# Performance work log

Measured on AMD Instinct MI355X. Metric: run time of the kernel, lower is better.

Reference implementation:

```python
import jax, jax.numpy as jnp
import numpy as np

B, N, E, Dh, L = 64, 128, 1024, 300, 2  # batch, num_utter, emb_dim, hidden_dim, gnn_layers


def gru_cell(x, h, wih, whh, bih, bhh):
    # torch.nn.GRUCell math; gate order r, z, n
    gi = x @ wih.T + bih
    gh = h @ whh.T + bhh
    ir, iz, inn = jnp.split(gi, 3, axis=-1)
    hr, hz, hn = jnp.split(gh, 3, axis=-1)
    r = jax.nn.sigmoid(ir + hr)
    z = jax.nn.sigmoid(iz + hz)
    n = jnp.tanh(inn + r * hn)
    return (1.0 - z) * n + z * h


def dag_layer(Hl, mask, wg, bg, cwih, cwhh, cbih, cbhh, pwih, pwhh, pbih, pbhh):
    # Hl: (B,N,Dh); mask: (B,N,N) strict-causal DAG adjacency (float 0/1)
    wq, wk = wg[:Dh], wg[Dh:]  # GatLinear: Linear(2*Dh, 1) split over [Q; K]
    x0 = Hl[:, 0]
    z0 = jnp.zeros_like(x0)
    C0 = gru_cell(x0, z0, cwih, cwhh, cbih, cbhh)  # grus_c(H0, hx=None)
    P0 = gru_cell(z0, x0, pwih, pwhh, pbih, pbhh)  # grus_p(M=0, H0)
    buf0 = jnp.zeros_like(Hl).at[:, 0].set(C0 + P0)

    xs = (jnp.swapaxes(Hl[:, 1:], 0, 1),      # (N-1,B,Dh)
          jnp.swapaxes(mask[:, 1:], 0, 1),    # (N-1,B,N)
          jnp.arange(1, Hl.shape[1]))

    def step(buf, inp):
        x, m, i = inp  # x:(B,Dh), m:(B,N) allows only positions j<i with adj==1
        alpha = (x @ wq)[:, None] + buf @ wk + bg        # (B,N) additive score
        alpha = alpha - (1.0 - m) * 1e30                 # mask_logic
        w = jax.nn.softmax(alpha, axis=-1)
        M = jnp.einsum('bn,bnd->bd', w, buf)             # attn_sum over history H1
        C = gru_cell(x, M, cwih, cwhh, cbih, cbhh)       # grus_c(H_i, M)
        P = gru_cell(M, x, pwih, pwhh, pbih, pbhh)       # grus_p(M, H_i)
        return buf.at[:, i].set(C + P), None

    buf, _ = jax.lax.scan(step, buf0, xs)
    return buf


def setup_inputs():
    key = jax.random.key(0)
    ks = jax.random.split(key, 16)
    features = jax.random.normal(ks[0], (B, N, E), jnp.float32)
    adj = jax.random.randint(ks[1], (B, N, N), 0, 2, dtype=jnp.int32)
    idx = jnp.arange(1, N)
    adj = adj.at[:, idx, idx - 1].set(1)  # every utterance links to its predecessor (valid DAG)
    s_mask = jax.random.randint(ks[2], (B, N, N), 0, 2, dtype=jnp.int32)
    s_mask_onehot = jax.nn.one_hot(s_mask, 2, dtype=jnp.int32)
    lengths = jnp.full((B,), N, dtype=jnp.int32)
    s = 0.05
    return {
        'features': features,
        'fc1_w': jax.random.normal(ks[3], (E, Dh), jnp.float32) * s,
        'fc1_b': jnp.zeros((Dh,), jnp.float32),
        'gat_w': jax.random.normal(ks[4], (L, 2 * Dh), jnp.float32) * s,
        'gat_b': jnp.zeros((L,), jnp.float32),
        'gc_wih': jax.random.normal(ks[5], (L, 3 * Dh, Dh), jnp.float32) * s,
        'gc_whh': jax.random.normal(ks[6], (L, 3 * Dh, Dh), jnp.float32) * s,
        'gc_bih': jnp.zeros((L, 3 * Dh), jnp.float32),
        'gc_bhh': jnp.zeros((L, 3 * Dh), jnp.float32),
        'gp_wih': jax.random.normal(ks[7], (L, 3 * Dh, Dh), jnp.float32) * s,
        'gp_whh': jax.random.normal(ks[8], (L, 3 * Dh, Dh), jnp.float32) * s,
        'gp_bih': jnp.zeros((L, 3 * Dh), jnp.float32),
        'gp_bhh': jnp.zeros((L, 3 * Dh), jnp.float32),
        'adj': adj,
        's_mask': s_mask,
        's_mask_onehot': s_mask_onehot,
        'lengths': lengths,
    }


def reference(features, fc1_w, fc1_b, gat_w, gat_b, gc_wih, gc_whh, gc_bih, gc_bhh,
              gp_wih, gp_whh, gp_bih, gp_bhh, adj, s_mask, s_mask_onehot, lengths):
    H0 = jax.nn.relu(features @ fc1_w + fc1_b)                 # (B,N,Dh)
    causal = jnp.tril(jnp.ones((N, N), features.dtype), k=-1)  # strictly past (j<i)
    mask = adj.astype(features.dtype) * causal                 # adj[:, i, :i]
    Hs = [H0]
    Hl = H0
    for l in range(L):
        Hl = dag_layer(Hl, mask, gat_w[l], gat_b[l],
                       gc_wih[l], gc_whh[l], gc_bih[l], gc_bhh[l],
                       gp_wih[l], gp_whh[l], gp_bih[l], gp_bhh[l])
        Hs.append(Hl)
    Hs.append(features)
    # nodal_att_type=None -> attentive_node_features is identity; module returns H
    return jnp.concatenate(Hs, axis=2)  # (B,N,Dh*(L+1)+E)
```

## Files before the change

### kernel.cpp

```cpp
#include <hip/hip_runtime.h>
#include <hip/hip_fp16.h>

#define B_   64
#define NB   128
#define E_   1024
#define DH   300
#define G3   900
#define OUTD 1924
#define SLICES 4
#define PK_STRIDE 1800
#define MROW 160

typedef _Float16 h2raw __attribute__((ext_vector_type(2)));

__device__ __forceinline__ float dot2f(unsigned int m2, unsigned int w, float acc) {
    h2raw a, b;
    __builtin_memcpy(&a, &m2, 4);
    __builtin_memcpy(&b, &w, 4);
    return __builtin_amdgcn_fdot2(a, b, acc, false);
}

__device__ __forceinline__ unsigned int packh2(float x, float y) {
    __half2 h;
    h.x = __float2half_rn(x);
    h.y = __float2half_rn(y);
    unsigned int u;
    __builtin_memcpy(&u, &h, 4);
    return u;
}

__device__ __forceinline__ float sigmoidf_(float x) { return 1.f / (1.f + __expf(-x)); }
__device__ __forceinline__ float tanh_fast(float x) { return 1.f - 2.f / (__expf(2.f * x) + 1.f); }

__global__ __launch_bounds__(256)
void copy_feat(const float* __restrict__ f, float* __restrict__ out) {
    const long id = (long)blockIdx.x * 256 + threadIdx.x;
    const long r = id >> 8;
    const int  c = (int)(id & 255);
    const float4 v = ((const float4*)(f + r * E_))[c];
    ((float4*)(out + r * OUTD + 3 * DH))[c] = v;
}

__global__ __launch_bounds__(256)
void pack2(const float* __restrict__ gc_whh, const float* __restrict__ gp_wih,
           unsigned int* __restrict__ dst) {
    const int id = blockIdx.x * 256 + threadIdx.x;
    if (id >= 2 * 150 * PK_STRIDE) return;
    const int l   = id / (150 * PK_STRIDE);
    const int rem = id % (150 * PK_STRIDE);
    const int kp  = rem / PK_STRIDE;
    const int R   = rem % PK_STRIDE;
    const int mat = R / G3;
    const int o   = R % G3;
    const float* W = (mat ? gp_wih : gc_whh) + (long)l * G3 * DH;
    const float2 v = *(const float2*)(W + (long)o * DH + 2 * kp);
    dst[id] = packh2(v.x, v.y);
}

__global__ __launch_bounds__(256)
void pack_af(const float* __restrict__ src, unsigned int* __restrict__ dst) {
    const long id = (long)blockIdx.x * 256 + threadIdx.x;
    const long r = id >> 9;
    const int kp = (int)(id & 511);
    const float2 v = *(const float2*)(src + r * E_ + 2 * kp);
    dst[id] = packh2(v.x, v.y);
}

__global__ __launch_bounds__(256)
void pack_ah(const float* __restrict__ src, unsigned int* __restrict__ dst) {
    const long id = (long)blockIdx.x * 256 + threadIdx.x;
    const long r = id / 160;
    const int kp = (int)(id % 160);
    unsigned int u = 0u;
    if (kp < 150) {
        const float2 v = *(const float2*)(src + r * OUTD + 2 * kp);
        u = packh2(v.x, v.y);
    }
    dst[id] = u;
}

__global__ __launch_bounds__(256)
void pack_bf(const float* __restrict__ W, unsigned int* __restrict__ dst) {
    const int id = blockIdx.x * 256 + threadIdx.x;
    const int n = id >> 9;
    const int kp = id & 511;
    unsigned int u = 0u;
    if (n < DH) u = packh2(W[(2 * kp) * DH + n], W[(2 * kp + 1) * DH + n]);
    dst[id] = u;
}

__global__ __launch_bounds__(256)
void pack_bw(const float* __restrict__ W, unsigned int* __restrict__ dst) {
    const int id = blockIdx.x * 256 + threadIdx.x;
    const int n = id / 160;
    const int kp = id % 160;
    unsigned int u = 0u;
    if (n < G3 && kp < 150) {
        const float2 v = *(const float2*)(W + (long)n * DH + 2 * kp);
        u = packh2(v.x, v.y);
    }
    dst[id] = u;
}

template<int RELU>
__global__ __launch_bounds__(256)
void gemm_h16(const unsigned int* __restrict__ APK, int ldap,
              const unsigned int* __restrict__ BPK, int ldbp,
              const float* __restrict__ bias,
              float* __restrict__ C, int ldc,
              int N, int KP)
{
    __shared__ __align__(16) unsigned int As[16][132];
    __shared__ __align__(16) unsigned int Bs[16][68];
    const int tid = threadIdx.x;
    const int m0 = blockIdx.y * 128;
    const int n0 = blockIdx.x * 64;
    const int tx = tid & 15, ty = tid >> 4;
    const int am = tid >> 1, ak8 = (tid & 1) * 8;
    const int bn = tid >> 2, bk4 = (tid & 3) * 4;

    float acc[8][4] = {{0.f}};
    const unsigned int* ap = APK + (long)(m0 + am) * ldap + ak8;
    const unsigned int* bp = BPK + (long)(n0 + bn) * ldbp + bk4;

    for (int kp0 = 0; kp0 < KP; kp0 += 16) {
        const uint4 a0 = *(const uint4*)(ap + kp0);
        const uint4 a1 = *(const uint4*)(ap + kp0 + 4);
        const uint4 bq = *(const uint4*)(bp + kp0);
        As[ak8 + 0][am] = a0.x; As[ak8 + 1][am] = a0.y;
        As[ak8 + 2][am] = a0.z; As[ak8 + 3][am] = a0.w;
        As[ak8 + 4][am] = a1.x; As[ak8 + 5][am] = a1.y;
        As[ak8 + 6][am] = a1.z; As[ak8 + 7][am] = a1.w;
        Bs[bk4 + 0][bn] = bq.x; Bs[bk4 + 1][bn] = bq.y;
        Bs[bk4 + 2][bn] = bq.z; Bs[bk4 + 3][bn] = bq.w;
        __syncthreads();
        #pragma unroll
        for (int kp = 0; kp < 16; ++kp) {
            const uint4 aA = *(const uint4*)&As[kp][ty * 8];
            const uint4 aB = *(const uint4*)&As[kp][ty * 8 + 4];
            const uint4 bb = *(const uint4*)&Bs[kp][tx * 4];
            const unsigned int av[8] = {aA.x, aA.y, aA.z, aA.w, aB.x, aB.y, aB.z, aB.w};
            const unsigned int bv[4] = {bb.x, bb.y, bb.z, bb.w};
            #pragma unroll
            for (int ii = 0; ii < 8; ++ii)
                #pragma unroll
                for (int jj = 0; jj < 4; ++jj)
                    acc[ii][jj] = dot2f(av[ii], bv[jj], acc[ii][jj]);
        }
        __syncthreads();
    }

    const int gn0 = n0 + tx * 4;
    #pragma unroll
    for (int ii = 0; ii < 8; ++ii) {
        const int gm = m0 + ty * 8 + ii;
        float* cp = C + (long)gm * ldc + gn0;
        if (gn0 + 3 < N) {
            const float4 bb = *(const float4*)&bias[gn0];
            float4 o;
            o.x = acc[ii][0] + bb.x; o.y = acc[ii][1] + bb.y;
            o.z = acc[ii][2] + bb.z; o.w = acc[ii][3] + bb.w;
            if (RELU) { o.x = fmaxf(o.x, 0.f); o.y = fmaxf(o.y, 0.f); o.z = fmaxf(o.z, 0.f); o.w = fmaxf(o.w, 0.f); }
            *(float4*)cp = o;
        } else if (gn0 < N) {
            for (int jj = 0; jj < 4; ++jj) {
                const int gn = gn0 + jj;
                if (gn < N) {
                    float v = acc[ii][jj] + bias[gn];
                    if (RELU) v = fmaxf(v, 0.f);
                    cp[jj] = v;
                }
            }
        }
    }
}

__global__ __launch_bounds__(512, 2)
void scan9(float* __restrict__ out,
           const float* __restrict__ GIC,
           const float* __restrict__ GHP,
           const unsigned int* __restrict__ PK2L,
           const float* __restrict__ cbhh,
           const float* __restrict__ pbih,
           const int* __restrict__ adj,
           const float* __restrict__ wk,
           unsigned long long* __restrict__ TBL,
           int l)
{
    extern __shared__ unsigned int histp[];
    __shared__ float wsm2[NB];
    __shared__ float betas[NB];
    __shared__ float Mlds[DH];
    __shared__ __align__(16) unsigned int M2[152];
    __shared__ float gmv[456];
    __shared__ float mx2s, S_pres;

    const int tid = threadIdx.x;
    const int lane = tid & 63;
    const int wid = tid >> 6;
    const int b = blockIdx.x & 63;
    const int k = blockIdx.x >> 6;
    const int swk = (k == 3) ? 72 : 76;

    float* outb = out + (long)b * NB * OUTD;
    const float* xcol = outb + l * DH;
    float* ycol = outb + (l + 1) * DH;
    const float* gicb = GIC + (long)b * NB * G3;
    const float* ghpb = GHP + (long)b * NB * G3;
    const int* adjb = adj + b * NB * NB;
    unsigned long long* mb = TBL + (long)b * NB * MROW;
    unsigned int* mb32 = (unsigned int*)mb;

    if (tid < 152) M2[tid] = 0u;

    const int D = 76 * k + ((tid < swk) ? tid : 0);
    const float cb0 = cbhh[D], cb1 = cbhh[DH + D], cb2 = cbhh[2 * DH + D];
    const float pb0 = pbih[D], pb1 = pbih[DH + D], pb2 = pbih[2 * DH + D];
    const float wkD = wk[D];

    const int ROWS = 6 * swk;
    int R;
    {
        const int t = (tid < ROWS) ? tid : 0;
        const int d = t % swk;
        const int r = t / swk;
        R = (r / 3) * G3 + (r % 3) * DH + 76 * k + d;
    }
    unsigned int w[152];
    #pragma unroll
    for (int j = 0; j < 150; ++j) w[j] = PK2L[j * PK_STRIDE + R];
    w[150] = 0u; w[151] = 0u;

    __syncthreads();

    const bool isv = (tid >= 256) && (tid < 406);
    const int vt = tid - 256;

    for (int i = 0; i < NB; ++i) {
        float gi0 = 0, gi1 = 0, gi2 = 0, gp0 = 0, gp1 = 0, gp2 = 0, xi = 0;
        if (tid < swk) {
            const float* gic = gicb + (long)i * G3;
            const float* ghp = ghpb + (long)i * G3;
            gi0 = gic[D]; gi1 = gic[DH + D]; gi2 = gic[2 * DH + D];
            gp0 = ghp[D]; gp1 = ghp[DH + D]; gp2 = ghp[2 * DH + D];
            xi = xcol[(long)i * OUTD + D];
        }
        int a0p = 0, a1p = 0;
        if (wid == 2 && i + 1 < NB) {
            a0p = adjb[(i + 1) * NB + lane];
            a1p = adjb[(i + 1) * NB + 64 + lane];
        }

        if (i > 0) {
            float V0 = 0.f, V1 = 0.f;
            if (wid == 0) {
                const unsigned long long* trow = mb + (long)(i - 1) * MROW;
                const unsigned int tag = (unsigned int)i;
                const bool act = (lane < 8);
                unsigned long long tv = 0;
                while (true) {
                    if (act && (unsigned int)tv != tag)
                        tv = __hip_atomic_load(&trow[152 + lane],
                                               __ATOMIC_RELAXED, __HIP_MEMORY_SCOPE_AGENT);
                    if (__all(!act || (unsigned int)tv == tag)) break;
                }
                float bp = 0.f;
                if (act) {
                    const unsigned int hb = (unsigned int)(tv >> 32);
                    __builtin_memcpy(&bp, &hb, 4);
                }
                bp += __shfl_xor(bp, 1);
                bp += __shfl_xor(bp, 2);
                bp += __shfl_xor(bp, 4);
                if (lane == 0) betas[i - 1] = __shfl(bp, 0);

                unsigned long long d0 = 0, d1 = 0;
                if (lane < 38) {
                    d0 = __hip_atomic_load(&trow[2 * lane],
                                           __ATOMIC_RELAXED, __HIP_MEMORY_SCOPE_AGENT);
                    d1 = __hip_atomic_load(&trow[2 * lane + 1],
                                           __ATOMIC_RELAXED, __HIP_MEMORY_SCOPE_AGENT);
                    uint4 q;
                    q.x = (unsigned int)d0; q.y = (unsigned int)(d0 >> 32);
                    q.z = (unsigned int)d1; q.w = (unsigned int)(d1 >> 32);
                    *(uint4*)&histp[(i - 1) * 152 + 4 * lane] = q;
                }
            } else if (isv) {
                #pragma unroll 4
                for (int j = 0; j + 1 < i; ++j) {
                    const float wj = wsm2[j];
                    const unsigned int u = histp[j * 152 + vt];
                    __half2 h; __builtin_memcpy(&h, &u, 4);
                    V0 = fmaf(wj, __half2float(h.x), V0);
                    V1 = fmaf(wj, __half2float(h.y), V1);
                }
            }
            __syncthreads();

            if (isv) {
                const float beta_new = betas[i - 1];
                const float mxl = mx2s;
                float S = S_pres, e;
                if (beta_new > mxl) {
                    const float sc = __expf(mxl - beta_new);
                    V0 *= sc; V1 *= sc; S *= sc; e = 1.f;
                } else {
                    e = __expf(beta_new - mxl);
                }
                const unsigned int u = histp[(i - 1) * 152 + vt];
                __half2 h; __builtin_memcpy(&h, &u, 4);
                S += e;
                V0 = fmaf(e, __half2float(h.x), V0);
                V1 = fmaf(e, __half2float(h.y), V1);
                const float inv = 1.f / S;
                const float m0 = V0 * inv, m1 = V1 * inv;
                Mlds[2 * vt] = m0;
                Mlds[2 * vt + 1] = m1;
                M2[vt] = packh2(m0, m1);
            }
        } else {
            if (tid < DH) Mlds[tid] = 0.f;
        }
        __syncthreads();

        if (tid < ROWS) {
            float a0 = 0.f, a1 = 0.f;
            #pragma unroll
            for (int j4 = 0; j4 < 152; j4 += 4) {
                const uint4 m4 = *(const uint4*)&M2[j4];
                a0 = dot2f(m4.x, w[j4 + 0], a0);
                a1 = dot2f(m4.y, w[j4 + 1], a1);
                a0 = dot2f(m4.z, w[j4 + 2], a0);
                a1 = dot2f(m4.w, w[j4 + 3], a1);
            }
            gmv[tid] = a0 + a1;
        }
        __syncthreads();

        if (wid < 2) {
            float rowv = 0.f;
            if (tid < swk) {
                const float Mi = Mlds[D];
                const float hc0 = gmv[0 * swk + tid] + cb0;
                const float hc1 = gmv[1 * swk + tid] + cb1;
                const float hc2 = gmv[2 * swk + tid] + cb2;
                const float rc = sigmoidf_(gi0 + hc0);
                const float zc = sigmoidf_(gi1 + hc1);
                const float nc = tanh_fast(gi2 + rc * hc2);
                const float Cc = (1.f - zc) * nc + zc * Mi;
                const float ip0 = gmv[3 * swk + tid] + pb0;
                const float ip1 = gmv[4 * swk + tid] + pb1;
                const float ip2 = gmv[5 * swk + tid] + pb2;
                const float rp = sigmoidf_(ip0 + gp0);
                const float zp = sigmoidf_(ip1 + gp1);
                const float np = tanh_fast(ip2 + rp * gp2);
                const float Pp = (1.f - zp) * np + zp * xi;
                rowv = Cc + Pp;
            }
            const float pr = __shfl_xor(rowv, 1);
            const unsigned int pairu32 = packh2(rowv, pr);
            if (tid < swk && !(tid & 1)) {
                __hip_atomic_store(&mb32[(long)i * (MROW * 2) + 38 * k + (tid >> 1)], pairu32,
                                   __ATOMIC_RELAXED, __HIP_MEMORY_SCOPE_AGENT);
            }
            float bv = (tid < swk) ? rowv * wkD : 0.f;
            #pragma unroll
            for (int off = 32; off; off >>= 1) bv += __shfl_xor(bv, off);
            asm volatile("s_waitcnt vmcnt(0)" ::: "memory");
            if (lane == 0) {
                unsigned int bbits;
                __builtin_memcpy(&bbits, &bv, 4);
                const unsigned long long pkt =
                    ((unsigned long long)bbits << 32) | (unsigned int)(i + 1);
                __hip_atomic_store(&mb[(long)i * MROW + 152 + 2 * k + wid], pkt,
                                   __ATOMIC_RELAXED, __HIP_MEMORY_SCOPE_AGENT);
            }
            if (tid < swk) ycol[(long)i * OUTD + D] = rowv;
        } else if (wid == 2 && i + 1 < NB) {
            const int j1 = lane + 64;
            const bool v0 = (lane < i) && (a0p != 0);
            const bool v1 = (j1 < i) && (a1p != 0);
            const float aa0 = v0 ? betas[lane] : -3.0e38f;
            const float aa1 = v1 ? betas[j1]   : -3.0e38f;
            float mx = fmaxf(aa0, aa1);
            #pragma unroll
            for (int off = 32; off; off >>= 1) mx = fmaxf(mx, __shfl_xor(mx, off));
            const float e0 = v0 ? __expf(aa0 - mx) : 0.f;
            const float e1 = v1 ? __expf(aa1 - mx) : 0.f;
            float s = e0 + e1;
            #pragma unroll
            for (int off = 32; off; off >>= 1) s += __shfl_xor(s, off);
            wsm2[lane] = e0;
            wsm2[j1]   = e1;
            if (lane == 0) { mx2s = mx; S_pres = s; }
        }
        __syncthreads();
    }
}

extern "C" void kernel_launch(void* const* d_in, const int* in_sizes, int n_in,
                              void* d_out, int out_size, void* d_ws, size_t ws_size,
                              hipStream_t stream) {
    (void)in_sizes; (void)n_in; (void)out_size; (void)ws_size;
    const float* features = (const float*)d_in[0];
    const float* fc1_w    = (const float*)d_in[1];
    const float* fc1_b    = (const float*)d_in[2];
    const float* gat_w    = (const float*)d_in[3];
    const float* gc_wih   = (const float*)d_in[5];
    const float* gc_whh   = (const float*)d_in[6];
    const float* gc_bih   = (const float*)d_in[7];
    const float* gc_bhh   = (const float*)d_in[8];
    const float* gp_wih   = (const float*)d_in[9];
    const float* gp_whh   = (const float*)d_in[10];
    const float* gp_bih   = (const float*)d_in[11];
    const float* gp_bhh   = (const float*)d_in[12];
    const int*   adj      = (const int*)d_in[13];
    float* out = (float*)d_out;

    unsigned long long* TB = (unsigned long long*)d_ws;
    float* GIC = (float*)(TB + 2L * B_ * NB * MROW);
    float* GHP = GIC + (long)B_ * NB * G3;
    unsigned int* PK2  = (unsigned int*)(GHP + (long)B_ * NB * G3);
    unsigned int* APK2 = PK2 + 2 * 150 * PK_STRIDE;
    unsigned int* BPKF = APK2 + 8192L * 160;
    unsigned int* BPKL = BPKF + 320L * 512;
    unsigned int* APK1 = (unsigned int*)GIC;

    hipFuncSetAttribute(reinterpret_cast<const void*>(scan9),
                        hipFuncAttributeMaxDynamicSharedMemorySize, 80000);
    hipMemsetAsync(TB, 0, 2L * B_ * NB * MROW * sizeof(unsigned long long), stream);

    copy_feat<<<dim3((B_ * NB * E_) / 1024), 256, 0, stream>>>(features, out);
    pack2<<<dim3((2 * 150 * PK_STRIDE + 255) / 256), 256, 0, stream>>>(gc_whh, gp_wih, PK2);

    pack_af<<<dim3(8192 * 512 / 256), 256, 0, stream>>>(features, APK1);
    pack_bf<<<dim3(320 * 512 / 256), 256, 0, stream>>>(fc1_w, BPKF);
    pack_bw<<<dim3(960 * 160 / 256), 256, 0, stream>>>(gc_wih,               BPKL + 0L * 153600);
    pack_bw<<<dim3(960 * 160 / 256), 256, 0, stream>>>(gp_whh,               BPKL + 1L * 153600);
    pack_bw<<<dim3(960 * 160 / 256), 256, 0, stream>>>(gc_wih + G3 * DH,     BPKL + 2L * 153600);
    pack_bw<<<dim3(960 * 160 / 256), 256, 0, stream>>>(gp_whh + G3 * DH,     BPKL + 3L * 153600);

    gemm_h16<1><<<dim3(5, 64), 256, 0, stream>>>(APK1, 512, BPKF, 512, fc1_b, out, OUTD, DH, 512);

    for (int l = 0; l < 2; ++l) {
        pack_ah<<<dim3(8192 * 160 / 256), 256, 0, stream>>>(out + l * DH, APK2);
        gemm_h16<0><<<dim3(15, 64), 256, 0, stream>>>(
            APK2, 160, BPKL + (2L * l) * 153600, 160, gc_bih + l * G3, GIC, G3, G3, 160);
        gemm_h16<0><<<dim3(15, 64), 256, 0, stream>>>(
            APK2, 160, BPKL + (2L * l + 1) * 153600, 160, gp_bhh + l * G3, GHP, G3, G3, 160);
        scan9<<<dim3(SLICES * B_), 512, 77824, stream>>>(
            out, GIC, GHP, PK2 + (long)l * 150 * PK_STRIDE,
            gc_bhh + l * G3, gp_bih + l * G3, adj,
            gat_w + l * 2 * DH + DH,
            TB + (long)l * B_ * NB * MROW, l);
    }
}
```

Before: 1.218 ms.

## Fuse layer-1 input GEMMs into layer-0 scan tail and transpose recurrent weights

The layer-0 scan kernel now gains a tail phase. It waits for the final history row, then computes the layer-1 input-gate and hidden-projection GEMMs from the fp16 history held in shared memory. The results go out as fp16 buffers, which replaces the separate pack_ah and two gemm_h16 launches for layer 1. The recurrent weights are repacked row-major with a padded stride so each thread loads its register weights as contiguous uint4 vectors instead of strided scalars. This removes launches and a global round trip, but it adds serial tail work per block, lowers precision of the layer-1 gate inputs to fp16, and drops the 2-blocks-per-CU launch bound.

```diff
diff --git a/kernel.cpp b/kernel.cpp
--- a/kernel.cpp
+++ b/kernel.cpp
@@ -8,8 +8,9 @@
 #define G3   900
 #define OUTD 1924
 #define SLICES 4
-#define PK_STRIDE 1800
 #define MROW 160
+#define WROW 152
+#define GSTRIDE 912
 
 typedef _Float16 h2raw __attribute__((ext_vector_type(2)));
 
@@ -42,19 +43,23 @@
 }
 
 __global__ __launch_bounds__(256)
-void pack2(const float* __restrict__ gc_whh, const float* __restrict__ gp_wih,
-           unsigned int* __restrict__ dst) {
+void pack2t(const float* __restrict__ gc_whh, const float* __restrict__ gp_wih,
+            unsigned int* __restrict__ dst) {
     const int id = blockIdx.x * 256 + threadIdx.x;
-    if (id >= 2 * 150 * PK_STRIDE) return;
-    const int l   = id / (150 * PK_STRIDE);
-    const int rem = id % (150 * PK_STRIDE);
-    const int kp  = rem / PK_STRIDE;
-    const int R   = rem % PK_STRIDE;
-    const int mat = R / G3;
-    const int o   = R % G3;
-    const float* W = (mat ? gp_wih : gc_whh) + (long)l * G3 * DH;
-    const float2 v = *(const float2*)(W + (long)o * DH + 2 * kp);
-    dst[id] = packh2(v.x, v.y);
+    if (id >= 2 * 1800 * WROW) return;
+    const int l   = id / (1800 * WROW);
+    const int rem = id % (1800 * WROW);
+    const int R   = rem / WROW;
+    const int kp  = rem % WROW;
+    unsigned int u = 0u;
+    if (kp < 150) {
+        const int mat = R / G3;
+        const int o   = R % G3;
+        const float* W = (mat ? gp_wih : gc_whh) + (long)l * G3 * DH;
+        const float2 v = *(const float2*)(W + (long)o * DH + 2 * kp);
+        u = packh2(v.x, v.y);
+    }
+    dst[id] = u;
 }
 
 __global__ __launch_bounds__(256)
@@ -175,17 +180,26 @@
     }
 }
 
-__global__ __launch_bounds__(512, 2)
-void scan9(float* __restrict__ out,
-           const float* __restrict__ GIC,
-           const float* __restrict__ GHP,
-           const unsigned int* __restrict__ PK2L,
-           const float* __restrict__ cbhh,
-           const float* __restrict__ pbih,
-           const int* __restrict__ adj,
-           const float* __restrict__ wk,
-           unsigned long long* __restrict__ TBL,
-           int l)
+__global__ __launch_bounds__(512)
+void scan10(float* __restrict__ out,
+            const float* __restrict__ GICf,
+            const float* __restrict__ GHPf,
+            const __half* __restrict__ GICh,
+            const __half* __restrict__ GHPh,
+            const unsigned int* __restrict__ PK2L,
+            const float* __restrict__ cbhh,
+            const float* __restrict__ pbih,
+            const int* __restrict__ adj,
+            const float* __restrict__ wk,
+            unsigned long long* __restrict__ TBL,
+            int l,
+            int do_tail,
+            const unsigned int* __restrict__ BW1c,
+            const unsigned int* __restrict__ BW1p,
+            const float* __restrict__ bih1,
+            const float* __restrict__ bhh1,
+            __half* __restrict__ G1C,
+            __half* __restrict__ G1P)
 {
     extern __shared__ unsigned int histp[];
     __shared__ float wsm2[NB];
@@ -205,8 +219,6 @@
     float* outb = out + (long)b * NB * OUTD;
     const float* xcol = outb + l * DH;
     float* ycol = outb + (l + 1) * DH;
-    const float* gicb = GIC + (long)b * NB * G3;
-    const float* ghpb = GHP + (long)b * NB * G3;
     const int* adjb = adj + b * NB * NB;
     unsigned long long* mb = TBL + (long)b * NB * MROW;
     unsigned int* mb32 = (unsigned int*)mb;
@@ -226,10 +238,12 @@
         const int r = t / swk;
         R = (r / 3) * G3 + (r % 3) * DH + 76 * k + d;
     }
-    unsigned int w[152];
-    #pragma unroll
-    for (int j = 0; j < 150; ++j) w[j] = PK2L[j * PK_STRIDE + R];
-    w[150] = 0u; w[151] = 0u;
+    uint4 wv[38];
+    {
+        const unsigned int* wrow = PK2L + (long)R * WROW;
+        #pragma unroll
+        for (int q = 0; q < 38; ++q) wv[q] = *(const uint4*)(wrow + 4 * q);
+    }
 
     __syncthreads();
 
@@ -239,10 +253,17 @@
     for (int i = 0; i < NB; ++i) {
         float gi0 = 0, gi1 = 0, gi2 = 0, gp0 = 0, gp1 = 0, gp2 = 0, xi = 0;
         if (tid < swk) {
-            const float* gic = gicb + (long)i * G3;
-            const float* ghp = ghpb + (long)i * G3;
-            gi0 = gic[D]; gi1 = gic[DH + D]; gi2 = gic[2 * DH + D];
-            gp0 = ghp[D]; gp1 = ghp[DH + D]; gp2 = ghp[2 * DH + D];
+            if (l == 0) {
+                const float* gic = GICf + ((long)b * NB + i) * G3;
+                const float* ghp = GHPf + ((long)b * NB + i) * G3;
+                gi0 = gic[D]; gi1 = gic[DH + D]; gi2 = gic[2 * DH + D];
+                gp0 = ghp[D]; gp1 = ghp[DH + D]; gp2 = ghp[2 * DH + D];
+            } else {
+                const __half* gic = GICh + ((long)b * NB + i) * GSTRIDE;
+                const __half* ghp = GHPh + ((long)b * NB + i) * GSTRIDE;
+                gi0 = __half2float(gic[D]); gi1 = __half2float(gic[DH + D]); gi2 = __half2float(gic[2 * DH + D]);
+                gp0 = __half2float(ghp[D]); gp1 = __half2float(ghp[DH + D]); gp2 = __half2float(ghp[2 * DH + D]);
+            }
             xi = xcol[(long)i * OUTD + D];
         }
         int a0p = 0, a1p = 0;
@@ -326,12 +347,12 @@
         if (tid < ROWS) {
             float a0 = 0.f, a1 = 0.f;
             #pragma unroll
-            for (int j4 = 0; j4 < 152; j4 += 4) {
-                const uint4 m4 = *(const uint4*)&M2[j4];
-                a0 = dot2f(m4.x, w[j4 + 0], a0);
-                a1 = dot2f(m4.y, w[j4 + 1], a1);
-                a0 = dot2f(m4.z, w[j4 + 2], a0);
-                a1 = dot2f(m4.w, w[j4 + 3], a1);
+            for (int q = 0; q < 38; ++q) {
+                const uint4 m4 = *(const uint4*)&M2[4 * q];
+                a0 = dot2f(m4.x, wv[q].x, a0);
+                a1 = dot2f(m4.y, wv[q].y, a1);
+                a0 = dot2f(m4.z, wv[q].z, a0);
+                a1 = dot2f(m4.w, wv[q].w, a1);
             }
             gmv[tid] = a0 + a1;
         }
@@ -396,6 +417,56 @@
         }
         __syncthreads();
     }
+
+    if (do_tail) {
+        if (wid == 0) {
+            const unsigned long long* trow = mb + 127L * MROW;
+            const unsigned int tag = 128u;
+            const bool act = (lane < 8);
+            unsigned long long tv = 0;
+            while (true) {
+                if (act && (unsigned int)tv != tag)
+                    tv = __hip_atomic_load(&trow[152 + lane],
+                                           __ATOMIC_RELAXED, __HIP_MEMORY_SCOPE_AGENT);
+                if (__all(!act || (unsigned int)tv == tag)) break;
+            }
+            if (lane < 38) {
+                const unsigned long long d0 = __hip_atomic_load(&trow[2 * lane],
+                                                  __ATOMIC_RELAXED, __HIP_MEMORY_SCOPE_AGENT);
+                const unsigned long long d1 = __hip_atomic_load(&trow[2 * lane + 1],
+                                                  __ATOMIC_RELAXED, __HIP_MEMORY_SCOPE_AGENT);
+                uint4 q;
+                q.x = (unsigned int)d0; q.y = (unsigned int)(d0 >> 32);
+                q.z = (unsigned int)d1; q.w = (unsigned int)(d1 >> 32);
+                *(uint4*)&histp[127 * 152 + 4 * lane] = q;
+            }
+        }
+        __syncthreads();
+
+        if (tid < 450) {
+            const int mat = tid / 225;
+            const int n = 225 * k + (tid % 225);
+            const unsigned int* brow = (mat ? BW1p : BW1c) + (long)n * 160;
+            uint4 bv[38];
+            #pragma unroll
+            for (int q = 0; q < 38; ++q) bv[q] = *(const uint4*)(brow + 4 * q);
+            const float bias = (mat ? bhh1 : bih1)[n];
+            __half* dsth = (mat ? G1P : G1C) + (long)b * NB * GSTRIDE + n;
+            for (int i = 0; i < NB; ++i) {
+                float a0 = 0.f, a1 = 0.f;
+                const unsigned int* arow = &histp[i * 152];
+                #pragma unroll
+                for (int q = 0; q < 38; ++q) {
+                    const uint4 m4 = *(const uint4*)(arow + 4 * q);
+                    a0 = dot2f(m4.x, bv[q].x, a0);
+                    a1 = dot2f(m4.y, bv[q].y, a1);
+                    a0 = dot2f(m4.z, bv[q].z, a0);
+                    a1 = dot2f(m4.w, bv[q].w, a1);
+                }
+                dsth[(long)i * GSTRIDE] = __float2half_rn(a0 + a1 + bias);
+            }
+        }
+    }
 }
 
 extern "C" void kernel_launch(void* const* d_in, const int* in_sizes, int n_in,
@@ -420,38 +491,50 @@
     unsigned long long* TB = (unsigned long long*)d_ws;
     float* GIC = (float*)(TB + 2L * B_ * NB * MROW);
     float* GHP = GIC + (long)B_ * NB * G3;
-    unsigned int* PK2  = (unsigned int*)(GHP + (long)B_ * NB * G3);
-    unsigned int* APK2 = PK2 + 2 * 150 * PK_STRIDE;
+    unsigned int* PK2T = (unsigned int*)(GHP + (long)B_ * NB * G3);
+    unsigned int* APK2 = PK2T + 2 * 1800 * WROW;
     unsigned int* BPKF = APK2 + 8192L * 160;
     unsigned int* BPKL = BPKF + 320L * 512;
+    __half* G1C = (__half*)(BPKL + 4L * 960 * 160);
+    __half* G1P = G1C + 8192L * GSTRIDE;
     unsigned int* APK1 = (unsigned int*)GIC;
 
-    hipFuncSetAttribute(reinterpret_cast<const void*>(scan9),
+    hipFuncSetAttribute(reinterpret_cast<const void*>(scan10),
                         hipFuncAttributeMaxDynamicSharedMemorySize, 80000);
     hipMemsetAsync(TB, 0, 2L * B_ * NB * MROW * sizeof(unsigned long long), stream);
 
     copy_feat<<<dim3((B_ * NB * E_) / 1024), 256, 0, stream>>>(features, out);
-    pack2<<<dim3((2 * 150 * PK_STRIDE + 255) / 256), 256, 0, stream>>>(gc_whh, gp_wih, PK2);
+    pack2t<<<dim3((2 * 1800 * WROW + 255) / 256), 256, 0, stream>>>(gc_whh, gp_wih, PK2T);
 
     pack_af<<<dim3(8192 * 512 / 256), 256, 0, stream>>>(features, APK1);
     pack_bf<<<dim3(320 * 512 / 256), 256, 0, stream>>>(fc1_w, BPKF);
-    pack_bw<<<dim3(960 * 160 / 256), 256, 0, stream>>>(gc_wih,               BPKL + 0L * 153600);
-    pack_bw<<<dim3(960 * 160 / 256), 256, 0, stream>>>(gp_whh,               BPKL + 1L * 153600);
-    pack_bw<<<dim3(960 * 160 / 256), 256, 0, stream>>>(gc_wih + G3 * DH,     BPKL + 2L * 153600);
-    pack_bw<<<dim3(960 * 160 / 256), 256, 0, stream>>>(gp_whh + G3 * DH,     BPKL + 3L * 153600);
+    pack_bw<<<dim3(960 * 160 / 256), 256, 0, stream>>>(gc_wih,           BPKL + 0L * 153600);
+    pack_bw<<<dim3(960 * 160 / 256), 256, 0, stream>>>(gp_whh,           BPKL + 1L * 153600);
+    pack_bw<<<dim3(960 * 160 / 256), 256, 0, stream>>>(gc_wih + G3 * DH, BPKL + 2L * 153600);
+    pack_bw<<<dim3(960 * 160 / 256), 256, 0, stream>>>(gp_whh + G3 * DH, BPKL + 3L * 153600);
 
     gemm_h16<1><<<dim3(5, 64), 256, 0, stream>>>(APK1, 512, BPKF, 512, fc1_b, out, OUTD, DH, 512);
 
-    for (int l = 0; l < 2; ++l) {
-        pack_ah<<<dim3(8192 * 160 / 256), 256, 0, stream>>>(out + l * DH, APK2);
-        gemm_h16<0><<<dim3(15, 64), 256, 0, stream>>>(
-            APK2, 160, BPKL + (2L * l) * 153600, 160, gc_bih + l * G3, GIC, G3, G3, 160);
-        gemm_h16<0><<<dim3(15, 64), 256, 0, stream>>>(
-            APK2, 160, BPKL + (2L * l + 1) * 153600, 160, gp_bhh + l * G3, GHP, G3, G3, 160);
-        scan9<<<dim3(SLICES * B_), 512, 77824, stream>>>(
-            out, GIC, GHP, PK2 + (long)l * 150 * PK_STRIDE,
-            gc_bhh + l * G3, gp_bih + l * G3, adj,
-            gat_w + l * 2 * DH + DH,
-            TB + (long)l * B_ * NB * MROW, l);
-    }
-}
+    pack_ah<<<dim3(8192 * 160 / 256), 256, 0, stream>>>(out, APK2);
+    gemm_h16<0><<<dim3(15, 64), 256, 0, stream>>>(
+        APK2, 160, BPKL + 0L * 153600, 160, gc_bih, GIC, G3, G3, 160);
+    gemm_h16<0><<<dim3(15, 64), 256, 0, stream>>>(
+        APK2, 160, BPKL + 1L * 153600, 160, gp_bhh, GHP, G3, G3, 160);
+
+    scan10<<<dim3(SLICES * B_), 512, 77824, stream>>>(
+        out, GIC, GHP, (const __half*)nullptr, (const __half*)nullptr,
+        PK2T + 0L * 1800 * WROW,
+        gc_bhh, gp_bih, adj, gat_w + DH,
+        TB, 0, 1,
+        BPKL + 2L * 153600, BPKL + 3L * 153600,
+        gc_bih + G3, gp_bhh + G3, G1C, G1P);
+
+    scan10<<<dim3(SLICES * B_), 512, 77824, stream>>>(
+        out, (const float*)nullptr, (const float*)nullptr, G1C, G1P,
+        PK2T + 1L * 1800 * WROW,
+        gc_bhh + G3, gp_bih + G3, adj, gat_w + 3 * DH,
+        TB + (long)B_ * NB * MROW, 1, 0,
+        (const unsigned int*)nullptr, (const unsigned int*)nullptr,
+        (const float*)nullptr, (const float*)nullptr,
+        (__half*)nullptr, (__half*)nullptr);
+}
```

New measurement: 2.083 ms. +71.0%, slower.

## Move scan GRU weights from registers to LDS plus global streaming

Applied to the files above, without the earlier changes.

The scan kernel no longer keeps 150 packed fp16 weight pairs per thread in registers. The first 42 k-pairs are staged once into LDS, and the remaining 108 are re-read from global memory on every time step inside the recurrent matvec. The aim is to relieve register pressure (spills and VGPR limits) in the sequential scan. The cost is extra LDS footprint, about 150 KB per block, which limits residency to one block per CU, plus repeated L2/global loads on the latency-critical serial path. M2 is also now read per element instead of as uint4 vectors.

```diff
diff --git a/kernel.cpp b/kernel.cpp
--- a/kernel.cpp
+++ b/kernel.cpp
@@ -10,6 +10,8 @@
 #define SLICES 4
 #define PK_STRIDE 1800
 #define MROW 160
+#define KP_LDS 42
+#define WL_STR 456
 
 typedef _Float16 h2raw __attribute__((ext_vector_type(2)));
 
@@ -176,18 +178,19 @@
 }
 
 __global__ __launch_bounds__(512, 2)
-void scan9(float* __restrict__ out,
-           const float* __restrict__ GIC,
-           const float* __restrict__ GHP,
-           const unsigned int* __restrict__ PK2L,
-           const float* __restrict__ cbhh,
-           const float* __restrict__ pbih,
-           const int* __restrict__ adj,
-           const float* __restrict__ wk,
-           unsigned long long* __restrict__ TBL,
-           int l)
+void scan11(float* __restrict__ out,
+            const float* __restrict__ GIC,
+            const float* __restrict__ GHP,
+            const unsigned int* __restrict__ PK2L,
+            const float* __restrict__ cbhh,
+            const float* __restrict__ pbih,
+            const int* __restrict__ adj,
+            const float* __restrict__ wk,
+            unsigned long long* __restrict__ TBL,
+            int l)
 {
     extern __shared__ unsigned int histp[];
+    unsigned int* wlds = histp + 128 * 152;
     __shared__ float wsm2[NB];
     __shared__ float betas[NB];
     __shared__ float Mlds[DH];
@@ -226,10 +229,20 @@
         const int r = t / swk;
         R = (r / 3) * G3 + (r % 3) * DH + 76 * k + d;
     }
-    unsigned int w[152];
-    #pragma unroll
-    for (int j = 0; j < 150; ++j) w[j] = PK2L[j * PK_STRIDE + R];
-    w[150] = 0u; w[151] = 0u;
+
+    for (int e = tid; e < KP_LDS * WL_STR; e += 512) {
+        const int kp = e / WL_STR;
+        const int rl = e % WL_STR;
+        unsigned int v = 0u;
+        if (rl < ROWS) {
+            const int mat  = rl / (3 * swk);
+            const int rest = rl % (3 * swk);
+            const int gate = rest / swk;
+            const int d    = rest % swk;
+            v = PK2L[kp * PK_STRIDE + mat * G3 + gate * DH + 76 * k + d];
+        }
+        wlds[e] = v;
+    }
 
     __syncthreads();
 
@@ -325,13 +338,17 @@
 
         if (tid < ROWS) {
             float a0 = 0.f, a1 = 0.f;
-            #pragma unroll
-            for (int j4 = 0; j4 < 152; j4 += 4) {
-                const uint4 m4 = *(const uint4*)&M2[j4];
-                a0 = dot2f(m4.x, w[j4 + 0], a0);
-                a1 = dot2f(m4.y, w[j4 + 1], a1);
-                a0 = dot2f(m4.z, w[j4 + 2], a0);
-                a1 = dot2f(m4.w, w[j4 + 3], a1);
+            const unsigned int* wg = PK2L + KP_LDS * PK_STRIDE + R;
+            #pragma unroll
+            for (int q = 0; q < 108; q += 2) {
+                a0 = dot2f(M2[KP_LDS + q],     wg[q * PK_STRIDE],       a0);
+                a1 = dot2f(M2[KP_LDS + q + 1], wg[(q + 1) * PK_STRIDE], a1);
+            }
+            const unsigned int* wl = wlds + tid;
+            #pragma unroll
+            for (int q = 0; q < KP_LDS; q += 2) {
+                a0 = dot2f(M2[q],     wl[q * WL_STR],       a0);
+                a1 = dot2f(M2[q + 1], wl[(q + 1) * WL_STR], a1);
             }
             gmv[tid] = a0 + a1;
         }
@@ -426,8 +443,9 @@
     unsigned int* BPKL = BPKF + 320L * 512;
     unsigned int* APK1 = (unsigned int*)GIC;
 
-    hipFuncSetAttribute(reinterpret_cast<const void*>(scan9),
-                        hipFuncAttributeMaxDynamicSharedMemorySize, 80000);
+    const int dynlds = (128 * 152 + KP_LDS * WL_STR) * 4;
+    hipFuncSetAttribute(reinterpret_cast<const void*>(scan11),
+                        hipFuncAttributeMaxDynamicSharedMemorySize, dynlds);
     hipMemsetAsync(TB, 0, 2L * B_ * NB * MROW * sizeof(unsigned long long), stream);
 
     copy_feat<<<dim3((B_ * NB * E_) / 1024), 256, 0, stream>>>(features, out);
@@ -435,10 +453,10 @@
 
     pack_af<<<dim3(8192 * 512 / 256), 256, 0, stream>>>(features, APK1);
     pack_bf<<<dim3(320 * 512 / 256), 256, 0, stream>>>(fc1_w, BPKF);
-    pack_bw<<<dim3(960 * 160 / 256), 256, 0, stream>>>(gc_wih,               BPKL + 0L * 153600);
-    pack_bw<<<dim3(960 * 160 / 256), 256, 0, stream>>>(gp_whh,               BPKL + 1L * 153600);
-    pack_bw<<<dim3(960 * 160 / 256), 256, 0, stream>>>(gc_wih + G3 * DH,     BPKL + 2L * 153600);
-    pack_bw<<<dim3(960 * 160 / 256), 256, 0, stream>>>(gp_whh + G3 * DH,     BPKL + 3L * 153600);
+    pack_bw<<<dim3(960 * 160 / 256), 256, 0, stream>>>(gc_wih,           BPKL + 0L * 153600);
+    pack_bw<<<dim3(960 * 160 / 256), 256, 0, stream>>>(gp_whh,           BPKL + 1L * 153600);
+    pack_bw<<<dim3(960 * 160 / 256), 256, 0, stream>>>(gc_wih + G3 * DH, BPKL + 2L * 153600);
+    pack_bw<<<dim3(960 * 160 / 256), 256, 0, stream>>>(gp_whh + G3 * DH, BPKL + 3L * 153600);
 
     gemm_h16<1><<<dim3(5, 64), 256, 0, stream>>>(APK1, 512, BPKF, 512, fc1_b, out, OUTD, DH, 512);
 
@@ -448,7 +466,7 @@
             APK2, 160, BPKL + (2L * l) * 153600, 160, gc_bih + l * G3, GIC, G3, G3, 160);
         gemm_h16<0><<<dim3(15, 64), 256, 0, stream>>>(
             APK2, 160, BPKL + (2L * l + 1) * 153600, 160, gp_bhh + l * G3, GHP, G3, G3, 160);
-        scan9<<<dim3(SLICES * B_), 512, 77824, stream>>>(
+        scan11<<<dim3(SLICES * B_), 512, dynlds, stream>>>(
             out, GIC, GHP, PK2 + (long)l * 150 * PK_STRIDE,
             gc_bhh + l * G3, gp_bih + l * G3, adj,
             gat_w + l * 2 * DH + DH,
```

New measurement: 2.112 ms. 1.73x slower.

## Split scan matvec reduction dimension across two thread halves with 1024-thread blocks

Applied to the files above, without the earlier changes.

The scan kernel now launches 1024 threads per block and splits each row's 150-element packed dot product into two halves handled by separate threads. Each thread holds 76 weight registers instead of 152, and the partial sums are added in the gate stage. This shortens the per-step serial matvec latency on the recurrence critical path and eases register pressure, at the cost of occupancy changing from 2x512 to 1x1024 threads and an extra LDS read per gate. It also issues the history atomic loads before the beta shuffle reduction so their latency overlaps.

```diff
diff --git a/kernel.cpp b/kernel.cpp
--- a/kernel.cpp
+++ b/kernel.cpp
@@ -175,24 +175,24 @@
     }
 }
 
-__global__ __launch_bounds__(512, 2)
-void scan9(float* __restrict__ out,
-           const float* __restrict__ GIC,
-           const float* __restrict__ GHP,
-           const unsigned int* __restrict__ PK2L,
-           const float* __restrict__ cbhh,
-           const float* __restrict__ pbih,
-           const int* __restrict__ adj,
-           const float* __restrict__ wk,
-           unsigned long long* __restrict__ TBL,
-           int l)
+__global__ __launch_bounds__(1024, 1)
+void scan13(float* __restrict__ out,
+            const float* __restrict__ GIC,
+            const float* __restrict__ GHP,
+            const unsigned int* __restrict__ PK2L,
+            const float* __restrict__ cbhh,
+            const float* __restrict__ pbih,
+            const int* __restrict__ adj,
+            const float* __restrict__ wk,
+            unsigned long long* __restrict__ TBL,
+            int l)
 {
     extern __shared__ unsigned int histp[];
     __shared__ float wsm2[NB];
     __shared__ float betas[NB];
     __shared__ float Mlds[DH];
     __shared__ __align__(16) unsigned int M2[152];
-    __shared__ float gmv[456];
+    __shared__ float gmv2[2 * 456];
     __shared__ float mx2s, S_pres;
 
     const int tid = threadIdx.x;
@@ -219,17 +219,22 @@
     const float wkD = wk[D];
 
     const int ROWS = 6 * swk;
+    const int mvt = (tid < 912) ? tid : 0;
+    const int mr = mvt % 456;
+    const int mh = mvt / 456;
     int R;
     {
-        const int t = (tid < ROWS) ? tid : 0;
+        const int t = (mr < ROWS) ? mr : 0;
         const int d = t % swk;
         const int r = t / swk;
         R = (r / 3) * G3 + (r % 3) * DH + 76 * k + d;
     }
-    unsigned int w[152];
+    unsigned int w[76];
     #pragma unroll
-    for (int j = 0; j < 150; ++j) w[j] = PK2L[j * PK_STRIDE + R];
-    w[150] = 0u; w[151] = 0u;
+    for (int j = 0; j < 76; ++j) {
+        const int kp = 76 * mh + j;
+        w[j] = (kp < 150) ? PK2L[kp * PK_STRIDE + R] : 0u;
+    }
 
     __syncthreads();
 
@@ -264,22 +269,24 @@
                                                __ATOMIC_RELAXED, __HIP_MEMORY_SCOPE_AGENT);
                     if (__all(!act || (unsigned int)tv == tag)) break;
                 }
-                float bp = 0.f;
-                if (act) {
-                    const unsigned int hb = (unsigned int)(tv >> 32);
-                    __builtin_memcpy(&bp, &hb, 4);
-                }
-                bp += __shfl_xor(bp, 1);
-                bp += __shfl_xor(bp, 2);
-                bp += __shfl_xor(bp, 4);
-                if (lane == 0) betas[i - 1] = __shfl(bp, 0);
-
                 unsigned long long d0 = 0, d1 = 0;
                 if (lane < 38) {
                     d0 = __hip_atomic_load(&trow[2 * lane],
                                            __ATOMIC_RELAXED, __HIP_MEMORY_SCOPE_AGENT);
                     d1 = __hip_atomic_load(&trow[2 * lane + 1],
                                            __ATOMIC_RELAXED, __HIP_MEMORY_SCOPE_AGENT);
+                }
+                float bp = 0.f;
+                if (act) {
+                    const unsigned int hb = (unsigned int)(tv >> 32);
+                    __builtin_memcpy(&bp, &hb, 4);
+                }
+                bp += __shfl_xor(bp, 1);
+                bp += __shfl_xor(bp, 2);
+                bp += __shfl_xor(bp, 4);
+                if (lane == 0) betas[i - 1] = __shfl(bp, 0);
+
+                if (lane < 38) {
                     uint4 q;
                     q.x = (unsigned int)d0; q.y = (unsigned int)(d0 >> 32);
                     q.z = (unsigned int)d1; q.w = (unsigned int)(d1 >> 32);
@@ -323,17 +330,17 @@
         }
         __syncthreads();
 
-        if (tid < ROWS) {
+        if (tid < 912) {
             float a0 = 0.f, a1 = 0.f;
             #pragma unroll
-            for (int j4 = 0; j4 < 152; j4 += 4) {
-                const uint4 m4 = *(const uint4*)&M2[j4];
-                a0 = dot2f(m4.x, w[j4 + 0], a0);
-                a1 = dot2f(m4.y, w[j4 + 1], a1);
-                a0 = dot2f(m4.z, w[j4 + 2], a0);
-                a1 = dot2f(m4.w, w[j4 + 3], a1);
-            }
-            gmv[tid] = a0 + a1;
+            for (int q = 0; q < 19; ++q) {
+                const uint4 m4 = *(const uint4*)&M2[76 * mh + 4 * q];
+                a0 = dot2f(m4.x, w[4 * q + 0], a0);
+                a1 = dot2f(m4.y, w[4 * q + 1], a1);
+                a0 = dot2f(m4.z, w[4 * q + 2], a0);
+                a1 = dot2f(m4.w, w[4 * q + 3], a1);
+            }
+            gmv2[456 * mh + mr] = a0 + a1;
         }
         __syncthreads();
 
@@ -341,16 +348,16 @@
             float rowv = 0.f;
             if (tid < swk) {
                 const float Mi = Mlds[D];
-                const float hc0 = gmv[0 * swk + tid] + cb0;
-                const float hc1 = gmv[1 * swk + tid] + cb1;
-                const float hc2 = gmv[2 * swk + tid] + cb2;
+                const float hc0 = gmv2[0 * swk + tid] + gmv2[456 + 0 * swk + tid] + cb0;
+                const float hc1 = gmv2[1 * swk + tid] + gmv2[456 + 1 * swk + tid] + cb1;
+                const float hc2 = gmv2[2 * swk + tid] + gmv2[456 + 2 * swk + tid] + cb2;
                 const float rc = sigmoidf_(gi0 + hc0);
                 const float zc = sigmoidf_(gi1 + hc1);
                 const float nc = tanh_fast(gi2 + rc * hc2);
                 const float Cc = (1.f - zc) * nc + zc * Mi;
-                const float ip0 = gmv[3 * swk + tid] + pb0;
-                const float ip1 = gmv[4 * swk + tid] + pb1;
-                const float ip2 = gmv[5 * swk + tid] + pb2;
+                const float ip0 = gmv2[3 * swk + tid] + gmv2[456 + 3 * swk + tid] + pb0;
+                const float ip1 = gmv2[4 * swk + tid] + gmv2[456 + 4 * swk + tid] + pb1;
+                const float ip2 = gmv2[5 * swk + tid] + gmv2[456 + 5 * swk + tid] + pb2;
                 const float rp = sigmoidf_(ip0 + gp0);
                 const float zp = sigmoidf_(ip1 + gp1);
                 const float np = tanh_fast(ip2 + rp * gp2);
@@ -426,7 +433,7 @@
     unsigned int* BPKL = BPKF + 320L * 512;
     unsigned int* APK1 = (unsigned int*)GIC;
 
-    hipFuncSetAttribute(reinterpret_cast<const void*>(scan9),
+    hipFuncSetAttribute(reinterpret_cast<const void*>(scan13),
                         hipFuncAttributeMaxDynamicSharedMemorySize, 80000);
     hipMemsetAsync(TB, 0, 2L * B_ * NB * MROW * sizeof(unsigned long long), stream);
 
@@ -435,10 +442,10 @@
 
     pack_af<<<dim3(8192 * 512 / 256), 256, 0, stream>>>(features, APK1);
     pack_bf<<<dim3(320 * 512 / 256), 256, 0, stream>>>(fc1_w, BPKF);
-    pack_bw<<<dim3(960 * 160 / 256), 256, 0, stream>>>(gc_wih,               BPKL + 0L * 153600);
-    pack_bw<<<dim3(960 * 160 / 256), 256, 0, stream>>>(gp_whh,               BPKL + 1L * 153600);
-    pack_bw<<<dim3(960 * 160 / 256), 256, 0, stream>>>(gc_wih + G3 * DH,     BPKL + 2L * 153600);
-    pack_bw<<<dim3(960 * 160 / 256), 256, 0, stream>>>(gp_whh + G3 * DH,     BPKL + 3L * 153600);
+    pack_bw<<<dim3(960 * 160 / 256), 256, 0, stream>>>(gc_wih,           BPKL + 0L * 153600);
+    pack_bw<<<dim3(960 * 160 / 256), 256, 0, stream>>>(gp_whh,           BPKL + 1L * 153600);
+    pack_bw<<<dim3(960 * 160 / 256), 256, 0, stream>>>(gc_wih + G3 * DH, BPKL + 2L * 153600);
+    pack_bw<<<dim3(960 * 160 / 256), 256, 0, stream>>>(gp_whh + G3 * DH, BPKL + 3L * 153600);
 
     gemm_h16<1><<<dim3(5, 64), 256, 0, stream>>>(APK1, 512, BPKF, 512, fc1_b, out, OUTD, DH, 512);
 
@@ -448,7 +455,7 @@
             APK2, 160, BPKL + (2L * l) * 153600, 160, gc_bih + l * G3, GIC, G3, G3, 160);
         gemm_h16<0><<<dim3(15, 64), 256, 0, stream>>>(
             APK2, 160, BPKL + (2L * l + 1) * 153600, 160, gp_bhh + l * G3, GHP, G3, G3, 160);
-        scan9<<<dim3(SLICES * B_), 512, 77824, stream>>>(
+        scan13<<<dim3(SLICES * B_), 1024, 77824, stream>>>(
             out, GIC, GHP, PK2 + (long)l * 150 * PK_STRIDE,
             gc_bhh + l * G3, gp_bih + l * G3, adj,
             gat_w + l * 2 * DH + DH,
```

New measurement: 1.445 ms. 1.19x slower.
